# Kernel tuning notes

Measured on AMD Instinct MI355X. Metric: run time of the kernel, lower is better.

## Reference

```python
import jax, jax.numpy as jnp
import numpy as np

N, D, H, O, E = 8192, 512, 2048, 512, 8

def setup_inputs() -> dict:
    key = jax.random.key(0)
    ks = jax.random.split(key, 7)
    s = lambda *sh: 1.0 / np.sqrt(sh[-2] if len(sh) > 1 else 1.0)
    x  = jax.random.normal(ks[0], (N, D), dtype=jnp.float32)
    Wr = jax.random.normal(ks[1], (D, E), dtype=jnp.float32) * (1.0 / np.sqrt(D))
    br = jnp.zeros((E,), dtype=jnp.float32)
    W1 = jax.random.normal(ks[2], (E, D, H), dtype=jnp.float32) * (1.0 / np.sqrt(D))
    b1 = jnp.zeros((E, H), dtype=jnp.float32)
    W2 = jax.random.normal(ks[3], (E, H, O), dtype=jnp.float32) * (1.0 / np.sqrt(H))
    b2 = jnp.zeros((E, O), dtype=jnp.float32)
    return {"x": x, "Wr": Wr, "br": br, "W1": W1, "b1": b1, "W2": W2, "b2": b2}


def reference(x, Wr, br, W1, b1, W2, b2):
    # --- supervised router step: Linear -> softmax -> max ---
    router_logits = x @ Wr + br                      # [N, E]
    router_probs = jax.nn.softmax(router_logits, axis=-1)
    p_max = jnp.max(router_probs, axis=-1)           # [N]
    routes = jnp.argmax(router_probs, axis=-1)       # [N] int
    onehot = jax.nn.one_hot(routes, W1.shape[0], dtype=x.dtype)  # [N, E] dispatch mask

    # --- per-expert MLP (dense reference for the gather/compute/scatter pattern) ---
    h = jax.nn.relu(jnp.einsum('nd,edh->enh', x, W1) + b1[:, None, :])  # [E, N, H]
    all_out = jnp.einsum('enh,eho->eno', h, W2) + b2[:, None, :]        # [E, N, O]

    # --- combine: each token takes its routed expert's output ---
    out = jnp.einsum('ne,eno->no', onehot, all_out)  # [N, O]

    # straight-through scaling: value 1 in fwd, routes gradient into router probs
    scale = p_max / jax.lax.stop_gradient(p_max)
    logits = out * scale[:, None]

    counts = jnp.sum(onehot, axis=0)                 # tokens per expert
    return logits, router_probs, counts
```

## Files before the change

### kernel.cpp

```cpp
#include <hip/hip_runtime.h>
#include <hip/hip_bf16.h>
#include <stdint.h>

#define N_TOK 8192
#define DIM   512
#define HID   2048
#define OUTD  512
#define NEXP  8

typedef short  bf16x8 __attribute__((ext_vector_type(8)));
typedef float  f32x4  __attribute__((ext_vector_type(4)));
typedef unsigned short u16x8 __attribute__((ext_vector_type(8)));

#define WS_CNT    0
#define WS_LIST   4096
#define WS_XBF    266240
#define WS_W1T    8654848
#define WS_W2T    25432064
#define WS_H      42209280

__device__ __forceinline__ unsigned short f2bf(float f) {
    uint32_t u = __builtin_bit_cast(uint32_t, f);
    u = (u + 0x7fffu + ((u >> 16) & 1u)) >> 16;
    return (unsigned short)u;
}

__device__ __forceinline__ void gload16(const void* g, void* l) {
    __builtin_amdgcn_global_load_lds(
        (const __attribute__((address_space(1))) unsigned int*)g,
        (__attribute__((address_space(3))) unsigned int*)l, 16, 0, 0);
}

#define MFMA_BF16 __builtin_amdgcn_mfma_f32_16x16x32_bf16

__global__ __launch_bounds__(256) void k1_kernel(
    const float* __restrict__ x, const float* __restrict__ wr, const float* __restrict__ br,
    const float* __restrict__ w1,
    float* __restrict__ probs, int* __restrict__ cnt, int* __restrict__ list,
    unsigned short* __restrict__ xbf, unsigned short* __restrict__ w1t)
{
    const int bid = blockIdx.x, tid = threadIdx.x;
    if (bid < 256) {
        __shared__ int lcnt[NEXP], lbase[NEXP];
        __shared__ int am_l[32], slot_l[32];
        const int w = tid >> 6, lane = tid & 63;
        if (tid < NEXP) lcnt[tid] = 0;
        __syncthreads();
        for (int i = 0; i < 8; i++) {
            const int n = bid * 32 + w * 8 + i;
            float acc[NEXP] = {};
            #pragma unroll
            for (int db = 0; db < 8; db++) {
                const int d = db * 64 + lane;
                const float xv = x[(size_t)n * DIM + d];
                const f32x4 wv0 = *(const f32x4*)&wr[d * 8];
                const f32x4 wv1 = *(const f32x4*)&wr[d * 8 + 4];
                #pragma unroll
                for (int e = 0; e < 4; e++) { acc[e] += xv * wv0[e]; acc[4 + e] += xv * wv1[e]; }
            }
            #pragma unroll
            for (int m = 1; m < 64; m <<= 1)
                #pragma unroll
                for (int e = 0; e < NEXP; e++) acc[e] += __shfl_xor(acc[e], m, 64);
            #pragma unroll
            for (int e = 0; e < NEXP; e++) acc[e] += br[e];
            float mx = acc[0]; int am = 0;
            #pragma unroll
            for (int e = 1; e < NEXP; e++) if (acc[e] > mx) { mx = acc[e]; am = e; }
            float p[NEXP]; float s = 0.f;
            #pragma unroll
            for (int e = 0; e < NEXP; e++) { p[e] = expf(acc[e] - mx); s += p[e]; }
            const float inv = 1.f / s;
            if (lane == 0) {
                f32x4 p0, p1;
                #pragma unroll
                for (int e = 0; e < 4; e++) { p0[e] = p[e] * inv; p1[e] = p[e + 4] * inv; }
                *(f32x4*)&probs[(size_t)n * NEXP]     = p0;
                *(f32x4*)&probs[(size_t)n * NEXP + 4] = p1;
                const int slot = atomicAdd(&lcnt[am], 1);
                am_l[w * 8 + i] = am; slot_l[w * 8 + i] = slot;
            }
        }
        __syncthreads();
        if (tid < NEXP) lbase[tid] = atomicAdd(&cnt[tid], lcnt[tid]);
        __syncthreads();
        if (tid < 32) {
            const int a = am_l[tid];
            list[a * N_TOK + lbase[a] + slot_l[tid]] = bid * 32 + tid;
        }
        const int row = bid * 32 + (tid >> 3), seg = tid & 7;
        const float* src = x + (size_t)row * DIM + seg * 64;
        unsigned short* dst = xbf + (size_t)row * DIM + seg * 64;
        #pragma unroll
        for (int j = 0; j < 8; j++) {
            f32x4 a = *(const f32x4*)&src[j * 8];
            f32x4 b = *(const f32x4*)&src[j * 8 + 4];
            u16x8 o;
            #pragma unroll
            for (int q2 = 0; q2 < 4; q2++) { o[q2] = f2bf(a[q2]); o[4 + q2] = f2bf(b[q2]); }
            *(u16x8*)&dst[j * 8] = o;
        }
    } else {
        __shared__ float t[64][65];
        const int loc = bid - 256, e = loc >> 8, l2 = loc & 255;
        const float* pin = w1 + (size_t)e * DIM * HID;
        unsigned short* pout = w1t + (size_t)e * DIM * HID;
        const int r0 = (l2 >> 5) * 64, c0 = (l2 & 31) * 64;
        const int r = tid >> 2, q = tid & 3;
        #pragma unroll
        for (int j = 0; j < 4; j++) {
            f32x4 v = *(const f32x4*)&pin[(size_t)(r0 + r) * HID + c0 + q * 16 + j * 4];
            #pragma unroll
            for (int i = 0; i < 4; i++) t[r][q * 16 + j * 4 + i] = v[i];
        }
        __syncthreads();
        unsigned short o[16];
        #pragma unroll
        for (int i = 0; i < 16; i++) o[i] = f2bf(t[q * 16 + i][r]);
        unsigned short* dst = &pout[(size_t)(c0 + r) * DIM + r0 + q * 16];
        *(u16x8*)dst       = *(const u16x8*)&o[0];
        *(u16x8*)(dst + 8) = *(const u16x8*)&o[8];
    }
}

__device__ __forceinline__ int xcd_swizzle(int bid, int nwg, bool& valid) {
    const int xcd = bid & 7, cidx = bid >> 3;
    const int q = nwg >> 3, r = nwg & 7;
    const int csz = q + (xcd < r ? 1 : 0);
    valid = (cidx < csz);
    return (xcd < r ? xcd * (q + 1) : r * (q + 1) + (xcd - r) * q) + cidx;
}

__device__ __forceinline__ void tile_map128(const int* __restrict__ cnt, int tile,
                                            int& e, int& row0, int& bs, int& m_e, int& ntiles) {
    int c[NEXP]; ntiles = 0;
    #pragma unroll
    for (int i = 0; i < NEXP; i++) { c[i] = cnt[i]; ntiles += (c[i] + 127) >> 7; }
    int t = tile, b = 0, ei = 0;
    #pragma unroll
    for (int i = 0; i < NEXP; i++) {
        const int nt = (c[i] + 127) >> 7;
        if (t >= 0 && t < nt) { ei = i; row0 = t << 7; bs = b; m_e = c[i]; }
        t -= nt; b += c[i];
    }
    e = ei;
}

#define G1_GRID 2272

__global__ __launch_bounds__(256) void gemmB_kernel(
    const unsigned short* __restrict__ xbf, const unsigned short* __restrict__ w1t,
    const float* __restrict__ b1, const int* __restrict__ list,
    const int* __restrict__ cnt, unsigned short* __restrict__ h,
    const float* __restrict__ w2, unsigned short* __restrict__ w2t)
{
    __shared__ char smem[25088] __attribute__((aligned(16)));
    const int tid = threadIdx.x;

    if ((int)blockIdx.x >= G1_GRID) {
        float (*t)[65] = (float(*)[65])smem;
        const int loc = blockIdx.x - G1_GRID, e = loc >> 8, l2 = loc & 255;
        const float* pin = w2 + (size_t)e * HID * OUTD;
        unsigned short* pout = w2t + (size_t)e * HID * OUTD;
        const int r0 = (l2 >> 3) * 64, c0 = (l2 & 7) * 64;
        const int r = tid >> 2, q = tid & 3;
        #pragma unroll
        for (int j = 0; j < 4; j++) {
            f32x4 v = *(const f32x4*)&pin[(size_t)(r0 + r) * OUTD + c0 + q * 16 + j * 4];
            #pragma unroll
            for (int i = 0; i < 4; i++) t[r][q * 16 + j * 4 + i] = v[i];
        }
        __syncthreads();
        unsigned short o[16];
        #pragma unroll
        for (int i = 0; i < 16; i++) o[i] = f2bf(t[q * 16 + i][r]);
        unsigned short* dst = &pout[(size_t)(c0 + r) * HID + r0 + q * 16];
        *(u16x8*)dst       = *(const u16x8*)&o[0];
        *(u16x8*)(dst + 8) = *(const u16x8*)&o[8];
        return;
    }

    unsigned short* ldsA = (unsigned short*)smem;
    unsigned short* ldsB = (unsigned short*)(smem + 16384);
    int* ldsTok = (int*)(smem + 24576);

    int e = 0, row0 = 0, bs = 0, m_e = 0, ntm = 0;
    tile_map128(cnt, 0, e, row0, bs, m_e, ntm);
    const int nwg = ntm * 32;
    bool valid; const int v = xcd_swizzle(blockIdx.x, nwg, valid);
    if (!valid) return;
    const int tile = v >> 5, ntile = v & 31;
    tile_map128(cnt, tile, e, row0, bs, m_e, ntm);
    const int n0 = ntile * 64;

    if (tid < 128) { int r = row0 + tid; if (r >= m_e) r = m_e - 1; ldsTok[tid] = list[e * N_TOK + r]; }
    __syncthreads();

    const int gslot = tid & 7;
    const unsigned short* aSrc[4]; const unsigned short* bSrc[2];
    #pragma unroll
    for (int i = 0; i < 4; i++) {
        const int row = (i * 256 + tid) >> 3;
        const int col = ((gslot ^ (row & 7)) << 3);
        aSrc[i] = xbf + (size_t)ldsTok[row] * DIM + col;
    }
    #pragma unroll
    for (int i = 0; i < 2; i++) {
        const int row = (i * 256 + tid) >> 3;
        const int col = ((gslot ^ (row & 7)) << 3);
        bSrc[i] = w1t + ((size_t)e * HID + n0 + row) * DIM + col;
    }

    f32x4 acc[4][2] = {};
    const int lane = tid & 63, wid = tid >> 6;
    const int wm = (wid >> 1) * 64, wn = (wid & 1) * 32;
    const int lrow = lane & 15, gk = lane >> 4, lm = lrow & 7;

    int rowA[4], rowB[2];
    #pragma unroll
    for (int f = 0; f < 4; f++) rowA[f] = (wm + f * 16 + lrow) * 64;
    #pragma unroll
    for (int f = 0; f < 2; f++) rowB[f] = (wn + f * 16 + lrow) * 64;

    for (int t = 0; t < 8; t++) {
        const int k0 = t * 64;
        __syncthreads();
        #pragma unroll
        for (int i = 0; i < 4; i++)
            gload16(aSrc[i] + k0, ldsA + ((i << 8) + (tid & 192)) * 8);
        #pragma unroll
        for (int i = 0; i < 2; i++)
            gload16(bSrc[i] + k0, ldsB + ((i << 8) + (tid & 192)) * 8);
        __syncthreads();
        #pragma unroll
        for (int kk = 0; kk < 2; kk++) {
            const int gsel = (((kk << 2) + gk) ^ lm) << 3;
            bf16x8 av[4], bv[2];
            #pragma unroll
            for (int f = 0; f < 4; f++)
                av[f] = *(const bf16x8*)&ldsA[rowA[f] + gsel];
            #pragma unroll
            for (int f = 0; f < 2; f++)
                bv[f] = *(const bf16x8*)&ldsB[rowB[f] + gsel];
            #pragma unroll
            for (int mf = 0; mf < 4; mf++)
                #pragma unroll
                for (int nf = 0; nf < 2; nf++)
                    acc[mf][nf] = MFMA_BF16(av[mf], bv[nf], acc[mf][nf], 0, 0, 0);
        }
    }

    const int hbase = bs + row0;
    float bias[2];
    #pragma unroll
    for (int nf = 0; nf < 2; nf++) bias[nf] = b1[e * HID + n0 + wn + nf * 16 + lrow];
    #pragma unroll
    for (int mf = 0; mf < 4; mf++) {
        #pragma unroll
        for (int j = 0; j < 4; j++) {
            const int m = wm + mf * 16 + gk * 4 + j;
            if (row0 + m < m_e) {
                const size_t ro = (size_t)(hbase + m) * HID + n0 + wn;
                #pragma unroll
                for (int nf = 0; nf < 2; nf++) {
                    float vv = acc[mf][nf][j] + bias[nf];
                    h[ro + nf * 16 + lrow] = f2bf(vv > 0.f ? vv : 0.f);
                }
            }
        }
    }
}

__global__ __launch_bounds__(256) void gemm2_kernel(
    const unsigned short* __restrict__ h, const unsigned short* __restrict__ w2t,
    const float* __restrict__ b2, const int* __restrict__ list,
    const int* __restrict__ cnt, float* __restrict__ out, float* __restrict__ counts)
{
    const int tid = threadIdx.x;
    if (blockIdx.x == 0 && tid < NEXP) counts[tid] = (float)cnt[tid];

    int e = 0, row0 = 0, bs = 0, m_e = 0, ntm = 0;
    tile_map128(cnt, 0, e, row0, bs, m_e, ntm);
    const int nwg = ntm * 8;
    bool valid; const int v = xcd_swizzle(blockIdx.x, nwg, valid);
    if (!valid) return;
    const int tile = v >> 3, ntile = v & 7;
    tile_map128(cnt, tile, e, row0, bs, m_e, ntm);
    const int n0 = ntile * 64;

    __shared__ unsigned short ldsA[128 * 128] __attribute__((aligned(16)));
    __shared__ unsigned short ldsB[64 * 128]  __attribute__((aligned(16)));
    __shared__ int ldsTok[128];
    if (tid < 128) { int r = row0 + tid; if (r >= m_e) r = m_e - 1; ldsTok[tid] = list[e * N_TOK + r]; }
    __syncthreads();

    const unsigned short* aSrc[8]; const unsigned short* bSrc[4];
    #pragma unroll
    for (int i = 0; i < 8; i++) {
        const int g = i * 256 + tid, row = g >> 4, gc = g & 15;
        int slot = row0 + row; if (slot >= m_e) slot = m_e - 1;
        aSrc[i] = h + (size_t)(bs + slot) * HID + ((gc ^ (row & 15)) << 3);
    }
    #pragma unroll
    for (int i = 0; i < 4; i++) {
        const int g = i * 256 + tid, row = g >> 4, gc = g & 15;
        bSrc[i] = w2t + ((size_t)e * OUTD + n0 + row) * HID + ((gc ^ (row & 15)) << 3);
    }

    f32x4 acc[4][2] = {};
    const int lane = tid & 63, wid = tid >> 6;
    const int wm = (wid >> 1) * 64, wn = (wid & 1) * 32;
    const int lrow = lane & 15, gk = lane >> 4;

    int rowA[4], rowB[2];
    #pragma unroll
    for (int f = 0; f < 4; f++) rowA[f] = (wm + f * 16 + lrow) * 128;
    #pragma unroll
    for (int f = 0; f < 2; f++) rowB[f] = (wn + f * 16 + lrow) * 128;

    for (int t = 0; t < 16; t++) {
        const int k0 = t * 128;
        __syncthreads();
        #pragma unroll
        for (int i = 0; i < 8; i++)
            gload16(aSrc[i] + k0, ldsA + (i * 256 + tid) * 8);
        #pragma unroll
        for (int i = 0; i < 4; i++)
            gload16(bSrc[i] + k0, ldsB + (i * 256 + tid) * 8);
        __syncthreads();
        #pragma unroll
        for (int kk = 0; kk < 4; kk++) {
            const int gsel = (((kk << 2) + gk) ^ lrow) << 3;
            bf16x8 av[4], bv[2];
            #pragma unroll
            for (int f = 0; f < 4; f++)
                av[f] = *(const bf16x8*)&ldsA[rowA[f] + gsel];
            #pragma unroll
            for (int f = 0; f < 2; f++)
                bv[f] = *(const bf16x8*)&ldsB[rowB[f] + gsel];
            #pragma unroll
            for (int mf = 0; mf < 4; mf++)
                #pragma unroll
                for (int nf = 0; nf < 2; nf++)
                    acc[mf][nf] = MFMA_BF16(av[mf], bv[nf], acc[mf][nf], 0, 0, 0);
        }
    }

    float bias[2];
    #pragma unroll
    for (int nf = 0; nf < 2; nf++) bias[nf] = b2[e * OUTD + n0 + wn + nf * 16 + lrow];
    #pragma unroll
    for (int mf = 0; mf < 4; mf++) {
        #pragma unroll
        for (int j = 0; j < 4; j++) {
            const int m = wm + mf * 16 + gk * 4 + j;
            if (row0 + m < m_e) {
                const size_t ro = (size_t)ldsTok[m] * OUTD + n0 + wn;
                #pragma unroll
                for (int nf = 0; nf < 2; nf++)
                    out[ro + nf * 16 + lrow] = acc[mf][nf][j] + bias[nf];
            }
        }
    }
}

extern "C" void kernel_launch(void* const* d_in, const int* in_sizes, int n_in,
                              void* d_out, int out_size, void* d_ws, size_t ws_size,
                              hipStream_t stream) {
    (void)in_sizes; (void)n_in; (void)out_size; (void)ws_size;
    const float* x  = (const float*)d_in[0];
    const float* wr = (const float*)d_in[1];
    const float* br = (const float*)d_in[2];
    const float* w1 = (const float*)d_in[3];
    const float* b1 = (const float*)d_in[4];
    const float* w2 = (const float*)d_in[5];
    const float* b2 = (const float*)d_in[6];

    float* out    = (float*)d_out;
    float* probs  = out + (size_t)N_TOK * OUTD;
    float* counts = probs + (size_t)N_TOK * NEXP;

    char* ws = (char*)d_ws;
    int* cnt     = (int*)(ws + WS_CNT);
    int* list    = (int*)(ws + WS_LIST);
    unsigned short* xbf = (unsigned short*)(ws + WS_XBF);
    unsigned short* w1t = (unsigned short*)(ws + WS_W1T);
    unsigned short* w2t = (unsigned short*)(ws + WS_W2T);
    unsigned short* hbf = (unsigned short*)(ws + WS_H);

    hipMemsetAsync(cnt, 0, NEXP * sizeof(int), stream);
    k1_kernel<<<2304, 256, 0, stream>>>(x, wr, br, w1, probs, cnt, list, xbf, w1t);
    gemmB_kernel<<<G1_GRID + 2048, 256, 0, stream>>>(xbf, w1t, b1, list, cnt, hbf, w2, w2t);
    gemm2_kernel<<<568, 256, 0, stream>>>(hbf, w2t, b2, list, cnt, out, counts);
}
```

Before: 101.5 us.

## Enlarge GEMM1 tiles to 128x256 with 512 threads and double-buffered LDS prefetch

Rewrites the first expert GEMM to use 512-thread workgroups computing 128x256 output tiles, with a double-buffered LDS pipeline. Global loads for the next K step are split across the two MFMA half-steps, and s_setprio is raised around the MFMA blocks. The fused W2 transpose path now handles two 64x64 tiles per workgroup. The goal is higher data reuse per tile and hiding global-load latency behind MFMA work. The cost is a much larger LDS footprint (about 97KB) per workgroup, which limits occupancy, and fewer workgroups overall.

```diff
diff --git a/kernel.cpp b/kernel.cpp
--- a/kernel.cpp
+++ b/kernel.cpp
@@ -146,123 +146,156 @@
     e = ei;
 }
 
-#define G1_GRID 2272
-
-__global__ __launch_bounds__(256) void gemmB_kernel(
+#define G1X_GRID 576
+
+__global__ __launch_bounds__(512) void gemm1x_kernel(
     const unsigned short* __restrict__ xbf, const unsigned short* __restrict__ w1t,
     const float* __restrict__ b1, const int* __restrict__ list,
     const int* __restrict__ cnt, unsigned short* __restrict__ h,
     const float* __restrict__ w2, unsigned short* __restrict__ w2t)
 {
-    __shared__ char smem[25088] __attribute__((aligned(16)));
+    __shared__ char smem[98816] __attribute__((aligned(16)));
     const int tid = threadIdx.x;
 
-    if ((int)blockIdx.x >= G1_GRID) {
-        float (*t)[65] = (float(*)[65])smem;
-        const int loc = blockIdx.x - G1_GRID, e = loc >> 8, l2 = loc & 255;
+    if ((int)blockIdx.x >= G1X_GRID) {
+        float (*t2)[64][65] = (float(*)[64][65])smem;
+        const int z = tid >> 8, tt = tid & 255;
+        const int tau = (blockIdx.x - G1X_GRID) * 2 + z;
+        const int e = tau >> 8, l2 = tau & 255;
         const float* pin = w2 + (size_t)e * HID * OUTD;
         unsigned short* pout = w2t + (size_t)e * HID * OUTD;
         const int r0 = (l2 >> 3) * 64, c0 = (l2 & 7) * 64;
-        const int r = tid >> 2, q = tid & 3;
+        const int r = tt >> 2, q = tt & 3;
         #pragma unroll
         for (int j = 0; j < 4; j++) {
             f32x4 v = *(const f32x4*)&pin[(size_t)(r0 + r) * OUTD + c0 + q * 16 + j * 4];
             #pragma unroll
-            for (int i = 0; i < 4; i++) t[r][q * 16 + j * 4 + i] = v[i];
+            for (int i = 0; i < 4; i++) t2[z][r][q * 16 + j * 4 + i] = v[i];
         }
         __syncthreads();
         unsigned short o[16];
         #pragma unroll
-        for (int i = 0; i < 16; i++) o[i] = f2bf(t[q * 16 + i][r]);
+        for (int i = 0; i < 16; i++) o[i] = f2bf(t2[z][q * 16 + i][r]);
         unsigned short* dst = &pout[(size_t)(c0 + r) * HID + r0 + q * 16];
         *(u16x8*)dst       = *(const u16x8*)&o[0];
         *(u16x8*)(dst + 8) = *(const u16x8*)&o[8];
         return;
     }
 
-    unsigned short* ldsA = (unsigned short*)smem;
-    unsigned short* ldsB = (unsigned short*)(smem + 16384);
-    int* ldsTok = (int*)(smem + 24576);
+    unsigned short (*ldsA)[8192]  = (unsigned short(*)[8192])smem;
+    unsigned short (*ldsB)[16384] = (unsigned short(*)[16384])(smem + 32768);
+    int* ldsTok = (int*)(smem + 98304);
 
     int e = 0, row0 = 0, bs = 0, m_e = 0, ntm = 0;
     tile_map128(cnt, 0, e, row0, bs, m_e, ntm);
-    const int nwg = ntm * 32;
+    const int nwg = ntm * 8;
     bool valid; const int v = xcd_swizzle(blockIdx.x, nwg, valid);
     if (!valid) return;
-    const int tile = v >> 5, ntile = v & 31;
+    const int tile = v >> 3, ntile = v & 7;
     tile_map128(cnt, tile, e, row0, bs, m_e, ntm);
-    const int n0 = ntile * 64;
+    const int n0 = ntile * 256;
 
     if (tid < 128) { int r = row0 + tid; if (r >= m_e) r = m_e - 1; ldsTok[tid] = list[e * N_TOK + r]; }
     __syncthreads();
 
     const int gslot = tid & 7;
-    const unsigned short* aSrc[4]; const unsigned short* bSrc[2];
+    const unsigned short* aSrc[2]; const unsigned short* bSrc[4];
+    #pragma unroll
+    for (int i = 0; i < 2; i++) {
+        const int row = (i * 512 + tid) >> 3;
+        aSrc[i] = xbf + (size_t)ldsTok[row] * DIM + ((gslot ^ (row & 7)) << 3);
+    }
     #pragma unroll
     for (int i = 0; i < 4; i++) {
-        const int row = (i * 256 + tid) >> 3;
-        const int col = ((gslot ^ (row & 7)) << 3);
-        aSrc[i] = xbf + (size_t)ldsTok[row] * DIM + col;
-    }
-    #pragma unroll
-    for (int i = 0; i < 2; i++) {
-        const int row = (i * 256 + tid) >> 3;
-        const int col = ((gslot ^ (row & 7)) << 3);
-        bSrc[i] = w1t + ((size_t)e * HID + n0 + row) * DIM + col;
-    }
-
-    f32x4 acc[4][2] = {};
+        const int row = (i * 512 + tid) >> 3;
+        bSrc[i] = w1t + ((size_t)e * HID + n0 + row) * DIM + ((gslot ^ (row & 7)) << 3);
+    }
+
+    f32x4 acc[4][4] = {};
     const int lane = tid & 63, wid = tid >> 6;
-    const int wm = (wid >> 1) * 64, wn = (wid & 1) * 32;
+    const int wr2 = wid >> 2, wc2 = wid & 3;
     const int lrow = lane & 15, gk = lane >> 4, lm = lrow & 7;
 
-    int rowA[4], rowB[2];
-    #pragma unroll
-    for (int f = 0; f < 4; f++) rowA[f] = (wm + f * 16 + lrow) * 64;
-    #pragma unroll
-    for (int f = 0; f < 2; f++) rowB[f] = (wn + f * 16 + lrow) * 64;
-
+    int rowA[4], rowB[4];
+    #pragma unroll
+    for (int f = 0; f < 4; f++) rowA[f] = (wr2 * 64 + f * 16 + lrow) * 64;
+    #pragma unroll
+    for (int f = 0; f < 4; f++) rowB[f] = (wc2 * 64 + f * 16 + lrow) * 64;
+
+    #pragma unroll
+    for (int i = 0; i < 2; i++) gload16(aSrc[i], &ldsA[0][(i * 512 + tid) * 8]);
+    #pragma unroll
+    for (int i = 0; i < 4; i++) gload16(bSrc[i], &ldsB[0][(i * 512 + tid) * 8]);
+    asm volatile("s_waitcnt vmcnt(0)" ::: "memory");
+    __builtin_amdgcn_sched_barrier(0);
+    __builtin_amdgcn_s_barrier();
+
+    #pragma unroll
     for (int t = 0; t < 8; t++) {
-        const int k0 = t * 64;
-        __syncthreads();
-        #pragma unroll
-        for (int i = 0; i < 4; i++)
-            gload16(aSrc[i] + k0, ldsA + ((i << 8) + (tid & 192)) * 8);
-        #pragma unroll
-        for (int i = 0; i < 2; i++)
-            gload16(bSrc[i] + k0, ldsB + ((i << 8) + (tid & 192)) * 8);
-        __syncthreads();
-        #pragma unroll
-        for (int kk = 0; kk < 2; kk++) {
-            const int gsel = (((kk << 2) + gk) ^ lm) << 3;
-            bf16x8 av[4], bv[2];
-            #pragma unroll
-            for (int f = 0; f < 4; f++)
-                av[f] = *(const bf16x8*)&ldsA[rowA[f] + gsel];
-            #pragma unroll
-            for (int f = 0; f < 2; f++)
-                bv[f] = *(const bf16x8*)&ldsB[rowB[f] + gsel];
+        const int buf = t & 1, nb = buf ^ 1, kn = (t + 1) * 64;
+        {
+            const int gsel = (gk ^ lm) << 3;
+            bf16x8 av[4], bv[4];
+            #pragma unroll
+            for (int f = 0; f < 4; f++) av[f] = *(const bf16x8*)&ldsA[buf][rowA[f] + gsel];
+            #pragma unroll
+            for (int f = 0; f < 4; f++) bv[f] = *(const bf16x8*)&ldsB[buf][rowB[f] + gsel];
+            if (t < 7) {
+                gload16(aSrc[0] + kn, &ldsA[nb][(0 * 512 + tid) * 8]);
+                gload16(aSrc[1] + kn, &ldsA[nb][(1 * 512 + tid) * 8]);
+                gload16(bSrc[0] + kn, &ldsB[nb][(0 * 512 + tid) * 8]);
+            }
+            __builtin_amdgcn_sched_barrier(0);
+            __builtin_amdgcn_s_setprio(1);
             #pragma unroll
             for (int mf = 0; mf < 4; mf++)
                 #pragma unroll
-                for (int nf = 0; nf < 2; nf++)
+                for (int nf = 0; nf < 4; nf++)
                     acc[mf][nf] = MFMA_BF16(av[mf], bv[nf], acc[mf][nf], 0, 0, 0);
+            __builtin_amdgcn_s_setprio(0);
+            __builtin_amdgcn_sched_barrier(0);
+            __builtin_amdgcn_s_barrier();
+        }
+        {
+            const int gsel = ((4 + gk) ^ lm) << 3;
+            bf16x8 av[4], bv[4];
+            #pragma unroll
+            for (int f = 0; f < 4; f++) av[f] = *(const bf16x8*)&ldsA[buf][rowA[f] + gsel];
+            #pragma unroll
+            for (int f = 0; f < 4; f++) bv[f] = *(const bf16x8*)&ldsB[buf][rowB[f] + gsel];
+            if (t < 7) {
+                gload16(bSrc[1] + kn, &ldsB[nb][(1 * 512 + tid) * 8]);
+                gload16(bSrc[2] + kn, &ldsB[nb][(2 * 512 + tid) * 8]);
+                gload16(bSrc[3] + kn, &ldsB[nb][(3 * 512 + tid) * 8]);
+            }
+            __builtin_amdgcn_sched_barrier(0);
+            __builtin_amdgcn_s_setprio(1);
+            #pragma unroll
+            for (int mf = 0; mf < 4; mf++)
+                #pragma unroll
+                for (int nf = 0; nf < 4; nf++)
+                    acc[mf][nf] = MFMA_BF16(av[mf], bv[nf], acc[mf][nf], 0, 0, 0);
+            __builtin_amdgcn_s_setprio(0);
+            __builtin_amdgcn_sched_barrier(0);
+            if (t < 7) asm volatile("s_waitcnt vmcnt(0)" ::: "memory");
+            __builtin_amdgcn_sched_barrier(0);
+            __builtin_amdgcn_s_barrier();
         }
     }
 
     const int hbase = bs + row0;
-    float bias[2];
-    #pragma unroll
-    for (int nf = 0; nf < 2; nf++) bias[nf] = b1[e * HID + n0 + wn + nf * 16 + lrow];
+    float bias[4];
+    #pragma unroll
+    for (int nf = 0; nf < 4; nf++) bias[nf] = b1[e * HID + n0 + wc2 * 64 + nf * 16 + lrow];
     #pragma unroll
     for (int mf = 0; mf < 4; mf++) {
         #pragma unroll
         for (int j = 0; j < 4; j++) {
-            const int m = wm + mf * 16 + gk * 4 + j;
+            const int m = wr2 * 64 + mf * 16 + gk * 4 + j;
             if (row0 + m < m_e) {
-                const size_t ro = (size_t)(hbase + m) * HID + n0 + wn;
-                #pragma unroll
-                for (int nf = 0; nf < 2; nf++) {
+                const size_t ro = (size_t)(hbase + m) * HID + n0 + wc2 * 64;
+                #pragma unroll
+                for (int nf = 0; nf < 4; nf++) {
                     float vv = acc[mf][nf][j] + bias[nf];
                     h[ro + nf * 16 + lrow] = f2bf(vv > 0.f ? vv : 0.f);
                 }
@@ -390,6 +423,6 @@
 
     hipMemsetAsync(cnt, 0, NEXP * sizeof(int), stream);
     k1_kernel<<<2304, 256, 0, stream>>>(x, wr, br, w1, probs, cnt, list, xbf, w1t);
-    gemmB_kernel<<<G1_GRID + 2048, 256, 0, stream>>>(xbf, w1t, b1, list, cnt, hbf, w2, w2t);
+    gemm1x_kernel<<<G1X_GRID + 1024, 512, 0, stream>>>(xbf, w1t, b1, list, cnt, hbf, w2, w2t);
     gemm2_kernel<<<568, 256, 0, stream>>>(hbf, w2t, b2, list, cnt, out, counts);
 }
```

New measurement: 112.9 us. +11.2%, slower.
